# Performance work log

Measured on AMD Instinct MI355X. Metric: run time of the kernel, lower is better.

The kernel has to match this reference:

```python
import jax, jax.numpy as jnp
import numpy as np

B, S, D, H, V = 4, 2048, 128, 4, 64
HD = D // H
ITERS = 3
SCALE = 1.0 / float(np.sqrt(HD))
APO = 0.2
TRP = 0.15
FC = 1.61803
EPS = 1e-5


def ln(x, g, b):
    m = x.mean(-1, keepdims=True)
    v = ((x - m) ** 2).mean(-1, keepdims=True)
    return (x - m) / jnp.sqrt(v + EPS) * g + b


def setup_inputs() -> dict:
    key = jax.random.key(0)
    ks = iter(jax.random.split(key, 64))

    def w(shape, s=0.02):
        return jax.random.normal(next(ks), shape, jnp.float32) * s

    return {
        "x": jax.random.normal(next(ks), (B, S, D), jnp.float32),
        "space": jax.random.normal(next(ks), (B, S, D), jnp.float32),
        # attn_norm
        "g_attn": jnp.ones(D), "b_attn": jnp.zeros(D),
        # RecursiveScaledDotProductAttention
        "Wq": w((D, D)), "Wk": w((D, D)), "Wv": w((D, D)),
        "Wo": w((D, D)), "bo": jnp.zeros(D),
        "Wg": w((D, 2 * D)), "bg": jnp.zeros(D),
        "Wobs": w((H, D)), "bobs": jnp.zeros(H),
        # trp_norm + TraumaResolutionPathLayer
        "g_trp": jnp.ones(D), "b_trp": jnp.zeros(D),
        "Wt": w((V, D)), "bt": jnp.zeros(V),
        "Wc": w((V, D)), "bc": jnp.zeros(V),
        "Ws": w((V, D)), "bs": jnp.zeros(V),
        "Wr": w((V, 3 * V)), "br": jnp.zeros(V),
        "fv": jnp.ones(V) * FC,
        "Wop": w((D, V)), "bop": jnp.zeros(D),
        # MorphogenesisFFN
        "g_ffn": jnp.ones(D), "b_ffn": jnp.zeros(D),
        "W1": w((4 * D, D)), "b1": jnp.zeros(4 * D),
        "W2": w((D, 4 * D)), "b2": jnp.zeros(D),
        "Wsg": w((D, D)), "bsg": jnp.zeros(D),
        # ApophasisLayer
        "g_apo": jnp.ones(D), "b_apo": jnp.zeros(D),
        "Wn": w((D, D)), "bn": jnp.zeros(D),
    }


def reference(x, space, g_attn, b_attn, Wq, Wk, Wv, Wo, bo, Wg, bg, Wobs, bobs,
              g_trp, b_trp, Wt, bt, Wc, bc, Ws, bs, Wr, br, fv, Wop, bop,
              g_ffn, b_ffn, W1, b1, W2, b2, Wsg, bsg, g_apo, b_apo, Wn, bn):
    # --- recursive attention (autopoiesis loop, eval mode: dropout = identity) ---
    xn = ln(x, g_attn, b_attn)
    obs = xn.mean(1, keepdims=True)                      # [B,1,D] observer_state default
    infl = (obs @ Wobs.T + bobs).transpose(0, 2, 1)[..., None]  # [B,H,1,1] per-head bias
    cur = xn
    for _ in range(ITERS):
        q = (cur @ Wq.T).reshape(B, S, H, HD).transpose(0, 2, 1, 3)
        k = (cur @ Wk.T).reshape(B, S, H, HD).transpose(0, 2, 1, 3)
        v = (cur @ Wv.T).reshape(B, S, H, HD).transpose(0, 2, 1, 3)
        scores = jnp.einsum('bhqd,bhkd->bhqk', q, k) * SCALE + infl
        aw = jax.nn.softmax(scores, axis=-1)             # [B,H,S,S]
        ao = jnp.einsum('bhqk,bhkd->bhqd', aw, v).transpose(0, 2, 1, 3).reshape(B, S, D)
        out = ao @ Wo.T + bo
        gate = jax.nn.sigmoid(jnp.concatenate([cur, out], -1) @ Wg.T + bg)
        cur = cur * (1 - gate) + out * gate
    x = x + cur
    # --- Trauma Resolution Path ---
    xn2 = ln(x, g_trp, b_trp)
    tv = xn2 @ Wt.T + bt                                 # [B,S,V]
    cv = jnp.broadcast_to(xn2.mean(1, keepdims=True) @ Wc.T + bc, tv.shape)
    sv = space @ Ws.T + bs
    rgate = jax.nn.sigmoid(jnp.concatenate([tv, cv, sv], -1) @ Wr.T + br)
    cn = jnp.maximum(jnp.linalg.norm(cv, axis=-1, keepdims=True), 1e-8)
    sn = jnp.maximum(jnp.linalg.norm(sv, axis=-1, keepdims=True), 1e-8)
    align = (cv * sv).sum(-1, keepdims=True) / (cn * sn)
    resolved = tv + TRP * (-align * (fv - tv) * rgate)
    x = x + resolved @ Wop.T + bop
    # --- Morphogenesis FFN ---
    xn3 = ln(x, g_ffn, b_ffn)
    ff = jax.nn.gelu(xn3 @ W1.T + b1, approximate=False) @ W2.T + b2
    x = x + jax.nn.sigmoid(xn3 @ Wsg.T + bsg) * ff
    # --- Apophasis ---
    x = x - APO * jnp.tanh(ln(x, g_apo, b_apo) @ Wn.T + bn)
    return x, aw
```

## Files before the change

kernel.cpp:

```cpp
#include <hip/hip_runtime.h>
#include <cstdint>
#include <cstddef>


typedef unsigned short u16;
typedef __attribute__((ext_vector_type(8))) short short8;
typedef __attribute__((ext_vector_type(4))) float f32x4;
typedef __attribute__((ext_vector_type(2))) unsigned uint32x2;

#define B_ 4
#define S_ 2048
#define D_ 128
#define H_ 4
#define M_ 8192
#define SCALE2_ 0.25503472510324417f
#define APO_ 0.2f
#define TRP_ 0.15f
#define EPS_ 1e-5f

__device__ __forceinline__ float fexp2(float x){ return __builtin_amdgcn_exp2f(x); }

__device__ __forceinline__ u16 f2bf(float f){
  unsigned u = __float_as_uint(f);
  unsigned r = ((u >> 16) & 1u) + 0x7fffu;
  return (u16)((u + r) >> 16);
}
__device__ __forceinline__ float bf2f(u16 u){ return __uint_as_float(((unsigned)u) << 16); }
__device__ __forceinline__ float sigm(float x){ return 1.0f/(1.0f + __expf(-x)); }

__device__ __forceinline__ unsigned cvtpk_bf16(float lo, float hi){
  unsigned r;
  asm("v_cvt_pk_bf16_f32 %0, %1, %2" : "=v"(r) : "v"(lo), "v"(hi));
  return r;
}

#define LDS_BARRIER() __asm__ volatile("s_waitcnt lgkmcnt(0)\n\ts_barrier" ::: "memory")

struct WSrc { const float* s[13]; };
__global__ __launch_bounds__(256) void prep_k(WSrc w, u16* __restrict__ dst,
    const float* __restrict__ x_in, const float* __restrict__ g,
    const float* __restrict__ b, u16* __restrict__ cg0){
  if (blockIdx.x < 1168){
    int idx = blockIdx.x*256 + threadIdx.x;
    if (idx >= 299008) return;
    const int sz[13] = {16384,16384,16384,16384,32768,8192,8192,12288,8192,65536,65536,16384,16384};
    int off = idx;
    #pragma unroll
    for (int seg = 0; seg < 13; ++seg){
      if (off < sz[seg]) { dst[idx] = f2bf(w.s[seg][off]); return; }
      off -= sz[seg];
    }
  } else {
    int wv = threadIdx.x >> 6, lane = threadIdx.x & 63;
    int row = (blockIdx.x - 1168)*4 + wv;
    size_t rb = (size_t)row * D_;
    float v0 = x_in[rb + lane], v1 = x_in[rb + lane + 64];
    float s = v0 + v1;
    #pragma unroll
    for (int m = 1; m < 64; m <<= 1) s += __shfl_xor(s, m, 64);
    float mean = s * (1.0f/128.0f);
    float d0 = v0 - mean, d1 = v1 - mean;
    float vv = d0*d0 + d1*d1;
    #pragma unroll
    for (int m = 1; m < 64; m <<= 1) vv += __shfl_xor(vv, m, 64);
    float rstd = rsqrtf(vv * (1.0f/128.0f) + EPS_);
    cg0[rb + lane]      = f2bf(d0*rstd*g[lane]    + b[lane]);
    cg0[rb + lane + 64] = f2bf(d1*rstd*g[lane+64] + b[lane+64]);
  }
}

__global__ __launch_bounds__(512) void colmean_k(const u16* __restrict__ lnb,
    const float* __restrict__ Wc, const float* __restrict__ bc,
    float* __restrict__ cv, float* __restrict__ cn){
  __shared__ float red2[32][128];
  __shared__ float cmS[128];
  int b = blockIdx.x;
  int tid = threadIdx.x;
  int rg = tid >> 4, c8 = (tid & 15)*8;
  const u16* pp = lnb + (size_t)b*S_*D_ + (size_t)rg*D_ + c8;
  float acc[8];
  #pragma unroll
  for (int j = 0; j < 8; ++j) acc[j] = 0.f;
  #pragma unroll 4
  for (int i = 0; i < 64; ++i){
    short8 v = *(const short8*)(pp + (size_t)i*32*D_);
    #pragma unroll
    for (int j = 0; j < 8; ++j) acc[j] += bf2f((u16)v[j]);
  }
  #pragma unroll
  for (int j = 0; j < 8; ++j) red2[rg][c8 + j] = acc[j];
  __syncthreads();
  if (tid < 128){
    float s = 0.f;
    #pragma unroll
    for (int r = 0; r < 32; ++r) s += red2[r][tid];
    cmS[tid] = s * (1.0f/2048.0f);
  }
  __syncthreads();
  if (tid < 64){
    int n = tid;
    const float* wrow = Wc + n*D_;
    float sacc = bc[n];
    #pragma unroll 4
    for (int dd = 0; dd < D_; ++dd) sacc += cmS[dd]*wrow[dd];
    cv[b*64 + n] = sacc;
    float sq = sacc*sacc;
    #pragma unroll
    for (int m = 1; m < 64; m <<= 1) sq += __shfl_xor(sq, m, 64);
    if (n == 0) cn[b] = fmaxf(sqrtf(sq), 1e-8f);
  }
}

__global__ __launch_bounds__(256) void gemm_qkv(const u16* __restrict__ A,
    const u16* __restrict__ W, u16* __restrict__ qh, u16* __restrict__ kh, u16* __restrict__ vt){
  __shared__ u16 Asm[64*136];
  __shared__ u16 Bsm[64*136];
  const int m0 = blockIdx.x*64, n0 = blockIdx.y*64;
  int tid = threadIdx.x;
  int wv = tid >> 6, lane = tid & 63, quad = lane >> 4, l15 = lane & 15;
  int wm = wv >> 1, wn = wv & 1;
  {
    int sr = tid >> 2, cb = (tid & 3)*32;
    const u16* ag = A + (size_t)(m0 + sr)*128 + cb;
    const u16* bg = W + (size_t)(n0 + sr)*128 + cb;
    short8 a0 = *(const short8*)(ag + 0);
    short8 a1 = *(const short8*)(ag + 8);
    short8 a2 = *(const short8*)(ag + 16);
    short8 a3 = *(const short8*)(ag + 24);
    short8 b0 = *(const short8*)(bg + 0);
    short8 b1 = *(const short8*)(bg + 8);
    short8 b2 = *(const short8*)(bg + 16);
    short8 b3 = *(const short8*)(bg + 24);
    *(short8*)(Asm + sr*136 + cb + 0)  = a0;
    *(short8*)(Asm + sr*136 + cb + 8)  = a1;
    *(short8*)(Asm + sr*136 + cb + 16) = a2;
    *(short8*)(Asm + sr*136 + cb + 24) = a3;
    *(short8*)(Bsm + sr*136 + cb + 0)  = b0;
    *(short8*)(Bsm + sr*136 + cb + 8)  = b1;
    *(short8*)(Bsm + sr*136 + cb + 16) = b2;
    *(short8*)(Bsm + sr*136 + cb + 24) = b3;
  }
  LDS_BARRIER();
  f32x4 acc[2][2];
  #pragma unroll
  for (int i = 0; i < 2; ++i)
    #pragma unroll
    for (int j = 0; j < 2; ++j) acc[i][j] = (f32x4){0.f,0.f,0.f,0.f};
  #pragma unroll
  for (int k0 = 0; k0 < 128; k0 += 32){
    short8 af0 = *(const short8*)(Asm + (wm*32      + l15)*136 + k0 + quad*8);
    short8 af1 = *(const short8*)(Asm + (wm*32 + 16 + l15)*136 + k0 + quad*8);
    short8 bf0 = *(const short8*)(Bsm + (wn*32      + l15)*136 + k0 + quad*8);
    short8 bf1 = *(const short8*)(Bsm + (wn*32 + 16 + l15)*136 + k0 + quad*8);
    acc[0][0] = __builtin_amdgcn_mfma_f32_16x16x32_bf16(af0, bf0, acc[0][0], 0,0,0);
    acc[0][1] = __builtin_amdgcn_mfma_f32_16x16x32_bf16(af0, bf1, acc[0][1], 0,0,0);
    acc[1][0] = __builtin_amdgcn_mfma_f32_16x16x32_bf16(af1, bf0, acc[1][0], 0,0,0);
    acc[1][1] = __builtin_amdgcn_mfma_f32_16x16x32_bf16(af1, bf1, acc[1][1], 0,0,0);
  }
  #pragma unroll
  for (int ms = 0; ms < 2; ++ms)
    #pragma unroll
    for (int ns = 0; ns < 2; ++ns){
      int mb = m0 + wm*32 + ms*16 + quad*4;
      int nn = n0 + wn*32 + ns*16 + l15;
      int which = nn >> 7, col = nn & 127, h = col >> 5, hd = col & 31;
      f32x4 c = acc[ms][ns];
      #pragma unroll
      for (int r = 0; r < 4; ++r){
        int m = mb + r, b = m >> 11, s = m & 2047;
        if (which == 0)      qh[((size_t)(b*H_+h)*S_ + s)*32 + hd] = f2bf(c[r]);
        else if (which == 1) kh[((size_t)(b*H_+h)*S_ + s)*32 + hd] = f2bf(c[r]);
        else                 vt[((size_t)(b*H_+h)*32 + hd)*S_ + s] = f2bf(c[r]);
      }
    }
}

template<bool WRITE_AW>
__global__ __launch_bounds__(256) void attn_k(const u16* __restrict__ qh, const u16* __restrict__ kh,
    const u16* __restrict__ vT, u16* __restrict__ ao_bf, float* __restrict__ aw){
  __shared__ u16 Ks[2][128*40];
  __shared__ u16 Vs[2][32*136];
  __shared__ u16 Ps[4*16*136];
  int L = blockIdx.y*32 + blockIdx.x;
  int xcd = L & 7, j = L >> 3;
  int bh = 2*xcd + (j >> 5);
  int q0 = (j & 31)*64;
  int b = bh >> 2, h = bh & 3;
  int tid = threadIdx.x, wv = tid >> 6, lane = tid & 63, quad = lane >> 4, l15 = lane & 15;
  int qrow = q0 + wv*16 + l15;
  const size_t bhS = (size_t)bh * S_;
  short8 qf = *(const short8*)(qh + (bhS + qrow)*32 + quad*8);
  int krow = tid >> 1, kseg = (tid & 1)*16;
  const u16* kg = kh + (bhS + krow)*32 + kseg;
  int vrow = tid >> 3, vseg = (tid & 7)*16;
  const u16* vg = vT + ((size_t)bh*32 + vrow)*S_ + vseg;
  f32x4 zero = {0.f,0.f,0.f,0.f};
  f32x4 ao0 = zero, ao1 = zero;
  float lsum = 0.f, rinv = 1.0f, nls = 0.f;
  u16* PsW = Ps + wv*16*136;

  if constexpr (WRITE_AW){
    {
      short8 a0 = *(const short8*)(kg + 0);
      short8 a1 = *(const short8*)(kg + 8);
      *(short8*)(Ks[0] + krow*40 + kseg    ) = a0;
      *(short8*)(Ks[0] + krow*40 + kseg + 8) = a1;
    }
    #pragma unroll 2
    for (int t = 0; t < 16; ++t){
      LDS_BARRIER();
      short8 n0, n1;
      if (t < 15){
        n0 = *(const short8*)(kg + (size_t)(t+1)*4096 + 0);
        n1 = *(const short8*)(kg + (size_t)(t+1)*4096 + 8);
      }
      const u16* Kb = Ks[t & 1];
      #pragma unroll
      for (int jt = 0; jt < 8; ++jt){
        short8 kf = *(const short8*)(Kb + (jt*16 + l15)*40 + quad*8);
        f32x4 s = __builtin_amdgcn_mfma_f32_16x16x32_bf16(kf, qf, zero, 0,0,0);
        #pragma unroll
        for (int r = 0; r < 4; ++r) lsum += fexp2(s[r]*SCALE2_);
      }
      if (t < 15){
        u16* Kn = Ks[(t+1) & 1];
        *(short8*)(Kn + krow*40 + kseg    ) = n0;
        *(short8*)(Kn + krow*40 + kseg + 8) = n1;
      }
    }
    lsum += __shfl_xor(lsum, 16, 64);
    lsum += __shfl_xor(lsum, 32, 64);
    nls = -__log2f(lsum);
  }

  {
    short8 a0 = *(const short8*)(kg + 0);
    short8 a1 = *(const short8*)(kg + 8);
    short8 b0 = *(const short8*)(vg + 0);
    short8 b1 = *(const short8*)(vg + 8);
    *(short8*)(Ks[0] + krow*40 + kseg    ) = a0;
    *(short8*)(Ks[0] + krow*40 + kseg + 8) = a1;
    *(short8*)(Vs[0] + vrow*136 + vseg    ) = b0;
    *(short8*)(Vs[0] + vrow*136 + vseg + 8) = b1;
  }
  #pragma unroll 2
  for (int t = 0; t < 16; ++t){
    LDS_BARRIER();
    short8 kn0, kn1, vn0, vn1;
    if (t < 15){
      kn0 = *(const short8*)(kg + (size_t)(t+1)*4096 + 0);
      kn1 = *(const short8*)(kg + (size_t)(t+1)*4096 + 8);
      vn0 = *(const short8*)(vg + (size_t)(t+1)*128 + 0);
      vn1 = *(const short8*)(vg + (size_t)(t+1)*128 + 8);
    }
    const u16* Kb = Ks[t & 1];
    const u16* Vb = Vs[t & 1];
    int k0 = t*128;
    #pragma unroll
    for (int jt = 0; jt < 8; ++jt){
      short8 kf = *(const short8*)(Kb + (jt*16 + l15)*40 + quad*8);
      f32x4 s = __builtin_amdgcn_mfma_f32_16x16x32_bf16(kf, qf, zero, 0,0,0);
      float pv[4];
      #pragma unroll
      for (int r = 0; r < 4; ++r){
        float e;
        if constexpr (WRITE_AW) e = fexp2(__builtin_fmaf(s[r], SCALE2_, nls));
        else { e = fexp2(s[r]*SCALE2_); lsum += e; }
        pv[r] = e;
      }
      if constexpr (WRITE_AW){
        f32x4 st = {pv[0], pv[1], pv[2], pv[3]};
        *(f32x4*)(aw + (bhS + qrow)*S_ + k0 + jt*16 + quad*4) = st;
      }
      uint32x2 pk;
      pk[0] = cvtpk_bf16(pv[0], pv[1]);
      pk[1] = cvtpk_bf16(pv[2], pv[3]);
      *(uint32x2*)(PsW + l15*136 + jt*16 + quad*4) = pk;
    }
    __asm__ volatile("s_waitcnt lgkmcnt(0)" ::: "memory");
    #pragma unroll
    for (int jg = 0; jg < 4; ++jg){
      short8 pf  = *(const short8*)(PsW + l15*136 + jg*32 + quad*8);
      short8 vf0 = *(const short8*)(Vb + (l15     )*136 + jg*32 + quad*8);
      short8 vf1 = *(const short8*)(Vb + (16 + l15)*136 + jg*32 + quad*8);
      ao0 = __builtin_amdgcn_mfma_f32_16x16x32_bf16(vf0, pf, ao0, 0,0,0);
      ao1 = __builtin_amdgcn_mfma_f32_16x16x32_bf16(vf1, pf, ao1, 0,0,0);
    }
    if (t < 15){
      u16* Kn = Ks[(t+1) & 1];
      u16* Vn = Vs[(t+1) & 1];
      *(short8*)(Kn + krow*40 + kseg    ) = kn0;
      *(short8*)(Kn + krow*40 + kseg + 8) = kn1;
      *(short8*)(Vn + vrow*136 + vseg    ) = vn0;
      *(short8*)(Vn + vrow*136 + vseg + 8) = vn1;
    }
  }

  if constexpr (!WRITE_AW){
    lsum += __shfl_xor(lsum, 16, 64);
    lsum += __shfl_xor(lsum, 32, 64);
    rinv = 1.0f / lsum;
  }

  size_t rowbase = ((size_t)(b*S_ + qrow))*D_ + h*32;
  #pragma unroll
  for (int dt = 0; dt < 2; ++dt){
    f32x4 a = dt ? ao1 : ao0;
    uint32x2 pk;
    pk[0] = cvtpk_bf16(a[0]*rinv, a[1]*rinv);
    pk[1] = cvtpk_bf16(a[2]*rinv, a[3]*rinv);
    *(uint32x2*)(ao_bf + rowbase + dt*16 + quad*4) = pk;
  }
}

template<bool DO_QKV>
__global__ __launch_bounds__(256) void wqkv_k(const u16* __restrict__ cin,
    const u16* __restrict__ ao_bf, const u16* __restrict__ wo, const u16* __restrict__ wg,
    const u16* __restrict__ w3, const float* __restrict__ bo, const float* __restrict__ bg,
    u16* __restrict__ cout, u16* __restrict__ qh, u16* __restrict__ kh, u16* __restrict__ vt,
    const float* __restrict__ x_in, const float* __restrict__ g_trp,
    const float* __restrict__ b_trp, float* __restrict__ xbuf, u16* __restrict__ lnb){
  __shared__ u16 aoS[16*136];
  __shared__ u16 cuS[16*136];
  __shared__ u16 outS[16*136];
  __shared__ u16 coS[16*136];
  const int m0 = blockIdx.x*16;
  int tid = threadIdx.x, wv = tid >> 6, lane = tid & 63, quad = lane >> 4, l15 = lane & 15;
  {
    int row = tid >> 4, seg = (tid & 15)*8;
    *(short8*)(aoS + row*136 + seg) = *(const short8*)(ao_bf + (size_t)(m0+row)*128 + seg);
    *(short8*)(cuS + row*136 + seg) = *(const short8*)(cin   + (size_t)(m0+row)*128 + seg);
  }
  __syncthreads();
  f32x4 oacc[2] = {(f32x4){0,0,0,0},(f32x4){0,0,0,0}};
  #pragma unroll
  for (int kc = 0; kc < 4; ++kc){
    short8 af = *(const short8*)(aoS + l15*136 + kc*32 + quad*8);
    #pragma unroll
    for (int nt = 0; nt < 2; ++nt){
      int n = wv*32 + nt*16 + l15;
      short8 bfv = *(const short8*)(wo + (size_t)n*128 + kc*32 + quad*8);
      oacc[nt] = __builtin_amdgcn_mfma_f32_16x16x32_bf16(af, bfv, oacc[nt], 0,0,0);
    }
  }
  #pragma unroll
  for (int nt = 0; nt < 2; ++nt){
    int n = wv*32 + nt*16 + l15;
    float bias = bo[n];
    #pragma unroll
    for (int r = 0; r < 4; ++r){
      int m = quad*4 + r;
      outS[m*136 + n] = f2bf(oacc[nt][r] + bias);
    }
  }
  __syncthreads();
  f32x4 gacc[2] = {(f32x4){0,0,0,0},(f32x4){0,0,0,0}};
  #pragma unroll
  for (int kc = 0; kc < 8; ++kc){
    short8 af = (kc < 4) ? *(const short8*)(cuS  + l15*136 + kc*32 + quad*8)
                         : *(const short8*)(outS + l15*136 + (kc-4)*32 + quad*8);
    #pragma unroll
    for (int nt = 0; nt < 2; ++nt){
      int n = wv*32 + nt*16 + l15;
      short8 bfv = *(const short8*)(wg + (size_t)n*256 + kc*32 + quad*8);
      gacc[nt] = __builtin_amdgcn_mfma_f32_16x16x32_bf16(af, bfv, gacc[nt], 0,0,0);
    }
  }
  #pragma unroll
  for (int nt = 0; nt < 2; ++nt){
    int n = wv*32 + nt*16 + l15;
    float biasg = bg[n], biaso = bo[n];
    #pragma unroll
    for (int r = 0; r < 4; ++r){
      int m = quad*4 + r;
      float g = sigm(gacc[nt][r] + biasg);
      float c = bf2f(cuS[m*136 + n]);
      float o = oacc[nt][r] + biaso;
      u16 val = f2bf(c + g*(o - c));
      coS[m*136 + n] = val;
      if constexpr (DO_QKV) cout[(size_t)(m0+m)*128 + n] = val;
    }
  }
  __syncthreads();
  if constexpr (DO_QKV){
    f32x4 qacc[6];
    #pragma unroll
    for (int i = 0; i < 6; ++i) qacc[i] = (f32x4){0,0,0,0};
    #pragma unroll
    for (int kc = 0; kc < 4; ++kc){
      short8 af = *(const short8*)(coS + l15*136 + kc*32 + quad*8);
      #pragma unroll
      for (int nt = 0; nt < 6; ++nt){
        int n = wv*96 + nt*16 + l15;
        short8 bfv = *(const short8*)(w3 + (size_t)n*128 + kc*32 + quad*8);
        qacc[nt] = __builtin_amdgcn_mfma_f32_16x16x32_bf16(af, bfv, qacc[nt], 0,0,0);
      }
    }
    #pragma unroll
    for (int nt = 0; nt < 6; ++nt){
      int nn = wv*96 + nt*16 + l15;
      int which = nn >> 7, col = nn & 127, h = col >> 5, hd = col & 31;
      #pragma unroll
      for (int r = 0; r < 4; ++r){
        int m = m0 + quad*4 + r, b = m >> 11, s = m & 2047;
        if (which == 0)      qh[((size_t)(b*H_+h)*S_ + s)*32 + hd] = f2bf(qacc[nt][r]);
        else if (which == 1) kh[((size_t)(b*H_+h)*S_ + s)*32 + hd] = f2bf(qacc[nt][r]);
        else                 vt[((size_t)(b*H_+h)*32 + hd)*S_ + s] = f2bf(qacc[nt][r]);
      }
    }
  } else {
    for (int rr = wv*4; rr < wv*4 + 4; ++rr){
      size_t rb = (size_t)(m0+rr)*128;
      float v0 = x_in[rb + lane]      + bf2f(coS[rr*136 + lane]);
      float v1 = x_in[rb + lane + 64] + bf2f(coS[rr*136 + lane + 64]);
      xbuf[rb + lane] = v0; xbuf[rb + lane + 64] = v1;
      float s = v0 + v1;
      #pragma unroll
      for (int m = 1; m < 64; m <<= 1) s += __shfl_xor(s, m, 64);
      float mean = s * (1.0f/128.0f);
      float d0 = v0 - mean, d1 = v1 - mean;
      float vv = d0*d0 + d1*d1;
      #pragma unroll
      for (int m = 1; m < 64; m <<= 1) vv += __shfl_xor(vv, m, 64);
      float rstd = rsqrtf(vv * (1.0f/128.0f) + EPS_);
      lnb[rb + lane]      = f2bf(d0*rstd*g_trp[lane]    + b_trp[lane]);
      lnb[rb + lane + 64] = f2bf(d1*rstd*g_trp[lane+64] + b_trp[lane+64]);
    }
  }
}

__global__ __launch_bounds__(256) void uber_k(const u16* __restrict__ lnb,
    const float* __restrict__ space, const float* __restrict__ xbuf,
    const float* __restrict__ cv, const float* __restrict__ cn,
    const u16* __restrict__ wt, const float* __restrict__ bt,
    const u16* __restrict__ wsx, const float* __restrict__ bs,
    const u16* __restrict__ wr, const float* __restrict__ br, const float* __restrict__ fv,
    const u16* __restrict__ wop, const float* __restrict__ bop,
    const float* __restrict__ g_ffn, const float* __restrict__ b_ffn,
    const u16* __restrict__ w1, const float* __restrict__ b1,
    const u16* __restrict__ w2, const float* __restrict__ b2,
    const u16* __restrict__ wsg, const float* __restrict__ bsg,
    const float* __restrict__ g_apo, const float* __restrict__ b_apo,
    const u16* __restrict__ wn, const float* __restrict__ bn,
    float* __restrict__ out_x){
  __shared__ u16 xnS[16*136];
  __shared__ u16 spS[16*136];
  __shared__ u16 CcS[16*200];
  __shared__ float svF[16*64];
  __shared__ u16 RsS[16*72];
  __shared__ float xrF[16*128];
  __shared__ u16 midS[16*536];
  __shared__ float alignS[16];
  const int m0 = blockIdx.x*16;
  const int bidx = m0 >> 11;
  int tid = threadIdx.x, wv = tid >> 6, lane = tid & 63, quad = lane >> 4, l15 = lane & 15;

  {
    int row = tid >> 4, seg = (tid & 15)*8;
    *(short8*)(xnS + row*136 + seg) = *(const short8*)(lnb + (size_t)(m0+row)*128 + seg);
    const float* sp = space + (size_t)(m0+row)*128 + seg;
    short8 pk;
    #pragma unroll
    for (int i = 0; i < 8; ++i) pk[i] = (short)f2bf(sp[i]);
    *(short8*)(spS + row*136 + seg) = pk;
    f32x4 xa = *(const f32x4*)(xbuf + (size_t)(m0+row)*128 + seg);
    f32x4 xb = *(const f32x4*)(xbuf + (size_t)(m0+row)*128 + seg + 4);
    *(f32x4*)(xrF + row*128 + seg) = xa;
    *(f32x4*)(xrF + row*128 + seg + 4) = xb;
  }
  __syncthreads();

  f32x4 tvacc = {0,0,0,0};
  {
    int n = wv*16 + l15;
    #pragma unroll
    for (int kc = 0; kc < 4; ++kc){
      short8 af  = *(const short8*)(xnS + l15*136 + kc*32 + quad*8);
      short8 bfv = *(const short8*)(wt + (size_t)n*128 + kc*32 + quad*8);
      tvacc = __builtin_amdgcn_mfma_f32_16x16x32_bf16(af, bfv, tvacc, 0,0,0);
    }
    float bias = bt[n];
    #pragma unroll
    for (int r = 0; r < 4; ++r){
      tvacc[r] += bias;
// ... 114 lines not shown
        int n = wv*128 + nt*16 + l15;
        short8 bfv = *(const short8*)(w1 + (size_t)n*128 + kc*32 + quad*8);
        acc[nt] = __builtin_amdgcn_mfma_f32_16x16x32_bf16(af, bfv, acc[nt], 0,0,0);
      }
    }
    #pragma unroll
    for (int nt = 0; nt < 8; ++nt){
      int n = wv*128 + nt*16 + l15;
      float bias = b1[n];
      #pragma unroll
      for (int r = 0; r < 4; ++r){
        int m = quad*4 + r;
        float lin = acc[nt][r] + bias;
        float ge = 0.5f*lin*(1.0f + erff(lin*0.70710678118654752f));
        midS[m*536 + n] = f2bf(ge);
      }
    }
  }
  __syncthreads();

  {
    f32x4 ffa[2] = {(f32x4){0,0,0,0},(f32x4){0,0,0,0}};
    #pragma unroll
    for (int kc = 0; kc < 16; ++kc){
      short8 af = *(const short8*)(midS + l15*536 + kc*32 + quad*8);
      #pragma unroll
      for (int nt = 0; nt < 2; ++nt){
        int n = wv*32 + nt*16 + l15;
        short8 bfv = *(const short8*)(w2 + (size_t)n*512 + kc*32 + quad*8);
        ffa[nt] = __builtin_amdgcn_mfma_f32_16x16x32_bf16(af, bfv, ffa[nt], 0,0,0);
      }
    }
    f32x4 sga[2] = {(f32x4){0,0,0,0},(f32x4){0,0,0,0}};
    #pragma unroll
    for (int kc = 0; kc < 4; ++kc){
      short8 af = *(const short8*)(xnS + l15*136 + kc*32 + quad*8);
      #pragma unroll
      for (int nt = 0; nt < 2; ++nt){
        int n = wv*32 + nt*16 + l15;
        short8 bfv = *(const short8*)(wsg + (size_t)n*128 + kc*32 + quad*8);
        sga[nt] = __builtin_amdgcn_mfma_f32_16x16x32_bf16(af, bfv, sga[nt], 0,0,0);
      }
    }
    #pragma unroll
    for (int nt = 0; nt < 2; ++nt){
      int n = wv*32 + nt*16 + l15;
      float b2n = b2[n], bsgn = bsg[n];
      #pragma unroll
      for (int r = 0; r < 4; ++r){
        int m = quad*4 + r;
        float ff = ffa[nt][r] + b2n;
        float sg = sigm(sga[nt][r] + bsgn);
        xrF[m*128 + n] += sg*ff;
      }
    }
  }
  __syncthreads();

  for (int rr = wv*4; rr < wv*4 + 4; ++rr){
    float v0 = xrF[rr*128 + lane], v1 = xrF[rr*128 + lane + 64];
    float s = v0 + v1;
    #pragma unroll
    for (int m = 1; m < 64; m <<= 1) s += __shfl_xor(s, m, 64);
    float mean = s * (1.0f/128.0f);
    float d0 = v0 - mean, d1 = v1 - mean;
    float vvv = d0*d0 + d1*d1;
    #pragma unroll
    for (int m = 1; m < 64; m <<= 1) vvv += __shfl_xor(vvv, m, 64);
    float rstd = rsqrtf(vvv * (1.0f/128.0f) + EPS_);
    xnS[rr*136 + lane]      = f2bf(d0*rstd*g_apo[lane]    + b_apo[lane]);
    xnS[rr*136 + lane + 64] = f2bf(d1*rstd*g_apo[lane+64] + b_apo[lane+64]);
  }
  __syncthreads();

  {
    f32x4 na[2] = {(f32x4){0,0,0,0},(f32x4){0,0,0,0}};
    #pragma unroll
    for (int kc = 0; kc < 4; ++kc){
      short8 af = *(const short8*)(xnS + l15*136 + kc*32 + quad*8);
      #pragma unroll
      for (int nt = 0; nt < 2; ++nt){
        int n = wv*32 + nt*16 + l15;
        short8 bfv = *(const short8*)(wn + (size_t)n*128 + kc*32 + quad*8);
        na[nt] = __builtin_amdgcn_mfma_f32_16x16x32_bf16(af, bfv, na[nt], 0,0,0);
      }
    }
    #pragma unroll
    for (int nt = 0; nt < 2; ++nt){
      int n = wv*32 + nt*16 + l15;
      float bias = bn[n];
      #pragma unroll
      for (int r = 0; r < 4; ++r){
        int m = quad*4 + r;
        out_x[(size_t)(m0+m)*128 + n] = xrF[m*128 + n] - APO_*tanhf(na[nt][r] + bias);
      }
    }
  }
}

extern "C" void kernel_launch(void* const* d_in, const int* in_sizes, int n_in,
                              void* d_out, int out_size, void* d_ws, size_t ws_size,
                              hipStream_t stream){
  (void)in_sizes; (void)n_in; (void)out_size; (void)ws_size;
  const float* x_in   = (const float*)d_in[0];
  const float* space  = (const float*)d_in[1];
  const float* g_attn = (const float*)d_in[2];
  const float* b_attn = (const float*)d_in[3];
  const float* Wq     = (const float*)d_in[4];
  const float* Wk     = (const float*)d_in[5];
  const float* Wv     = (const float*)d_in[6];
  const float* Wo     = (const float*)d_in[7];
  const float* bo     = (const float*)d_in[8];
  const float* Wg     = (const float*)d_in[9];
  const float* bg     = (const float*)d_in[10];
  const float* g_trp  = (const float*)d_in[13];
  const float* b_trp  = (const float*)d_in[14];
  const float* Wt     = (const float*)d_in[15];
  const float* bt     = (const float*)d_in[16];
  const float* Wc     = (const float*)d_in[17];
  const float* bc     = (const float*)d_in[18];
  const float* Ws_    = (const float*)d_in[19];
  const float* bs     = (const float*)d_in[20];
  const float* Wr     = (const float*)d_in[21];
  const float* br     = (const float*)d_in[22];
  const float* fv     = (const float*)d_in[23];
  const float* Wop    = (const float*)d_in[24];
  const float* bop    = (const float*)d_in[25];
  const float* g_ffn  = (const float*)d_in[26];
  const float* b_ffn  = (const float*)d_in[27];
  const float* W1_    = (const float*)d_in[28];
  const float* b1     = (const float*)d_in[29];
  const float* W2_    = (const float*)d_in[30];
  const float* b2     = (const float*)d_in[31];
  const float* Wsg_   = (const float*)d_in[32];
  const float* bsg    = (const float*)d_in[33];
  const float* g_apo  = (const float*)d_in[34];
  const float* b_apo  = (const float*)d_in[35];
  const float* Wn_    = (const float*)d_in[36];
  const float* bn     = (const float*)d_in[37];

  char* base = (char*)d_ws;
  size_t off = 0;
  auto alloc = [&](size_t bytes)->char* {
    char* r = base + off; off += (bytes + 255) & ~(size_t)255; return r; };
  u16*  wbf   = (u16*) alloc((size_t)299008*2);
  u16*  cg0   = (u16*) alloc((size_t)M_*D_*2);
  u16*  cg1   = (u16*) alloc((size_t)M_*D_*2);
  u16*  qh    = (u16*) alloc((size_t)16*S_*32*2);
  u16*  kh    = (u16*) alloc((size_t)16*S_*32*2);
  u16*  vt    = (u16*) alloc((size_t)16*32*S_*2);
  u16*  ao_bf = (u16*) alloc((size_t)M_*D_*2);
  u16*  lnb   = (u16*) alloc((size_t)M_*D_*2);
  float* xbuf = (float*)alloc((size_t)M_*D_*4);
  float* cvb  = (float*)alloc(4*64*4);
  float* cnb  = (float*)alloc(4*4);

  u16* wqkv = wbf;
  u16* wo   = wbf + 49152;
  u16* wg   = wbf + 65536;
  u16* wt   = wbf + 98304;
  u16* wsx  = wbf + 106496;
  u16* wr   = wbf + 114688;
  u16* wop  = wbf + 126976;
  u16* w1   = wbf + 135168;
  u16* w2   = wbf + 200704;
  u16* wsgp = wbf + 266240;
  u16* wn   = wbf + 282624;

  float* out_x = (float*)d_out;
  float* aw    = out_x + (size_t)M_*D_;

  WSrc wsrc;
  wsrc.s[0]=Wq; wsrc.s[1]=Wk; wsrc.s[2]=Wv; wsrc.s[3]=Wo; wsrc.s[4]=Wg;
  wsrc.s[5]=Wt; wsrc.s[6]=Ws_; wsrc.s[7]=Wr; wsrc.s[8]=Wop; wsrc.s[9]=W1_;
  wsrc.s[10]=W2_; wsrc.s[11]=Wsg_; wsrc.s[12]=Wn_;

  prep_k<<<1168 + M_/4, 256, 0, stream>>>(wsrc, wbf, x_in, g_attn, b_attn, cg0);
  gemm_qkv<<<dim3(M_/64, 6), 256, 0, stream>>>(cg0, wqkv, qh, kh, vt);

  attn_k<false><<<dim3(S_/64, 16), 256, 0, stream>>>(qh, kh, vt, ao_bf, nullptr);
  wqkv_k<true ><<<M_/16, 256, 0, stream>>>(cg0, ao_bf, wo, wg, wqkv, bo, bg, cg1, qh, kh, vt,
                                           x_in, g_trp, b_trp, xbuf, lnb);
  attn_k<false><<<dim3(S_/64, 16), 256, 0, stream>>>(qh, kh, vt, ao_bf, nullptr);
  wqkv_k<true ><<<M_/16, 256, 0, stream>>>(cg1, ao_bf, wo, wg, wqkv, bo, bg, cg0, qh, kh, vt,
                                           x_in, g_trp, b_trp, xbuf, lnb);
  attn_k<true ><<<dim3(S_/64, 16), 256, 0, stream>>>(qh, kh, vt, ao_bf, aw);
  wqkv_k<false><<<M_/16, 256, 0, stream>>>(cg0, ao_bf, wo, wg, wqkv, bo, bg, cg1, qh, kh, vt,
                                           x_in, g_trp, b_trp, xbuf, lnb);

  colmean_k<<<4, 512, 0, stream>>>(lnb, Wc, bc, cvb, cnb);

  uber_k<<<M_/16, 256, 0, stream>>>(lnb, space, xbuf, cvb, cnb,
      wt, bt, wsx, bs, wr, br, fv, wop, bop,
      g_ffn, b_ffn, w1, b1, w2, b2, wsgp, bsg,
      g_apo, b_apo, wn, bn, out_x);
}
```

Before: 214.1 us.

## Fuse weight conversion, input layernorm and first QKV GEMM into one kernel

Merges the prep kernel (fp32→bf16 weight conversion plus the attention layernorm) with the first QKV projection GEMM into a single launch. Each GEMM block computes the layernorm for its 64 rows directly into shared memory and converts its Wq/Wk/Wv slice from fp32 on the fly. A seventh grid row handles the remaining weight conversion with a grid-stride loop. This removes one launch and the round trip of cg0 and the bf16 QKV weights through global memory, at the cost of redundant layernorm work across the six column blocks. It also adds an LDS barrier in the attention kernel after the log-sum pass, apparently to fix a shared-memory reuse hazard.

```diff
diff --git a/kernel.cpp b/kernel.cpp
--- a/kernel.cpp
+++ b/kernel.cpp
@@ -37,23 +37,35 @@
 #define LDS_BARRIER() __asm__ volatile("s_waitcnt lgkmcnt(0)\n\ts_barrier" ::: "memory")
 
 struct WSrc { const float* s[13]; };
-__global__ __launch_bounds__(256) void prep_k(WSrc w, u16* __restrict__ dst,
-    const float* __restrict__ x_in, const float* __restrict__ g,
-    const float* __restrict__ b, u16* __restrict__ cg0){
-  if (blockIdx.x < 1168){
-    int idx = blockIdx.x*256 + threadIdx.x;
-    if (idx >= 299008) return;
+
+__global__ __launch_bounds__(256) void qkv0_k(WSrc w, u16* __restrict__ wbf,
+    const float* __restrict__ x_in, const float* __restrict__ g, const float* __restrict__ b,
+    u16* __restrict__ cg0, u16* __restrict__ qh, u16* __restrict__ kh, u16* __restrict__ vt){
+  if (blockIdx.y == 6){
     const int sz[13] = {16384,16384,16384,16384,32768,8192,8192,12288,8192,65536,65536,16384,16384};
-    int off = idx;
-    #pragma unroll
-    for (int seg = 0; seg < 13; ++seg){
-      if (off < sz[seg]) { dst[idx] = f2bf(w.s[seg][off]); return; }
-      off -= sz[seg];
-    }
-  } else {
-    int wv = threadIdx.x >> 6, lane = threadIdx.x & 63;
-    int row = (blockIdx.x - 1168)*4 + wv;
-    size_t rb = (size_t)row * D_;
+    for (int idx = blockIdx.x*256 + threadIdx.x; idx < 299008; idx += 128*256){
+      int off = idx;
+      const float* src = nullptr;
+      #pragma unroll
+      for (int seg = 0; seg < 13; ++seg){
+        if (src == nullptr){
+          if (off < sz[seg]) src = w.s[seg] + off;
+          else off -= sz[seg];
+        }
+      }
+      wbf[idx] = f2bf(*src);
+    }
+    return;
+  }
+  __shared__ u16 Asm[64*136];
+  __shared__ u16 Bsm[64*136];
+  const int m0 = blockIdx.x*64, n0 = blockIdx.y*64;
+  int tid = threadIdx.x;
+  int wv = tid >> 6, lane = tid & 63, quad = lane >> 4, l15 = lane & 15;
+  int wm = wv >> 1, wn = wv & 1;
+
+  for (int rr = wv*16; rr < wv*16 + 16; ++rr){
+    size_t rb = (size_t)(m0 + rr) * D_;
     float v0 = x_in[rb + lane], v1 = x_in[rb + lane + 64];
     float s = v0 + v1;
     #pragma unroll
@@ -64,9 +76,63 @@
     #pragma unroll
     for (int m = 1; m < 64; m <<= 1) vv += __shfl_xor(vv, m, 64);
     float rstd = rsqrtf(vv * (1.0f/128.0f) + EPS_);
-    cg0[rb + lane]      = f2bf(d0*rstd*g[lane]    + b[lane]);
-    cg0[rb + lane + 64] = f2bf(d1*rstd*g[lane+64] + b[lane+64]);
-  }
+    u16 o0 = f2bf(d0*rstd*g[lane]    + b[lane]);
+    u16 o1 = f2bf(d1*rstd*g[lane+64] + b[lane+64]);
+    Asm[rr*136 + lane]      = o0;
+    Asm[rr*136 + lane + 64] = o1;
+    if (n0 == 0){ cg0[rb + lane] = o0; cg0[rb + lane + 64] = o1; }
+  }
+  {
+    int sr = tid >> 2, cb = (tid & 3)*32;
+    int gr = n0 + sr;
+    const float* wsrc = (gr < 128) ? (w.s[0] + (size_t)gr*128)
+                      : (gr < 256) ? (w.s[1] + (size_t)(gr-128)*128)
+                                   : (w.s[2] + (size_t)(gr-256)*128);
+    #pragma unroll
+    for (int j = 0; j < 32; j += 8){
+      f32x4 fa = *(const f32x4*)(wsrc + cb + j);
+      f32x4 fb = *(const f32x4*)(wsrc + cb + j + 4);
+      short8 pk;
+      pk[0]=(short)f2bf(fa[0]); pk[1]=(short)f2bf(fa[1]);
+      pk[2]=(short)f2bf(fa[2]); pk[3]=(short)f2bf(fa[3]);
+      pk[4]=(short)f2bf(fb[0]); pk[5]=(short)f2bf(fb[1]);
+      pk[6]=(short)f2bf(fb[2]); pk[7]=(short)f2bf(fb[3]);
+      *(short8*)(Bsm + sr*136 + cb + j) = pk;
+    }
+  }
+  LDS_BARRIER();
+  f32x4 acc[2][2];
+  #pragma unroll
+  for (int i = 0; i < 2; ++i)
+    #pragma unroll
+    for (int j = 0; j < 2; ++j) acc[i][j] = (f32x4){0.f,0.f,0.f,0.f};
+  #pragma unroll
+  for (int k0 = 0; k0 < 128; k0 += 32){
+    short8 af0 = *(const short8*)(Asm + (wm*32      + l15)*136 + k0 + quad*8);
+    short8 af1 = *(const short8*)(Asm + (wm*32 + 16 + l15)*136 + k0 + quad*8);
+    short8 bf0 = *(const short8*)(Bsm + (wn*32      + l15)*136 + k0 + quad*8);
+    short8 bf1 = *(const short8*)(Bsm + (wn*32 + 16 + l15)*136 + k0 + quad*8);
+    acc[0][0] = __builtin_amdgcn_mfma_f32_16x16x32_bf16(af0, bf0, acc[0][0], 0,0,0);
+    acc[0][1] = __builtin_amdgcn_mfma_f32_16x16x32_bf16(af0, bf1, acc[0][1], 0,0,0);
+    acc[1][0] = __builtin_amdgcn_mfma_f32_16x16x32_bf16(af1, bf0, acc[1][0], 0,0,0);
+    acc[1][1] = __builtin_amdgcn_mfma_f32_16x16x32_bf16(af1, bf1, acc[1][1], 0,0,0);
+  }
+  #pragma unroll
+  for (int ms = 0; ms < 2; ++ms)
+    #pragma unroll
+    for (int ns = 0; ns < 2; ++ns){
+      int mb = m0 + wm*32 + ms*16 + quad*4;
+      int nn = n0 + wn*32 + ns*16 + l15;
+      int which = nn >> 7, col = nn & 127, h = col >> 5, hd = col & 31;
+      f32x4 c = acc[ms][ns];
+      #pragma unroll
+      for (int r = 0; r < 4; ++r){
+        int m = mb + r, b2 = m >> 11, s = m & 2047;
+        if (which == 0)      qh[((size_t)(b2*H_+h)*S_ + s)*32 + hd] = f2bf(c[r]);
+        else if (which == 1) kh[((size_t)(b2*H_+h)*S_ + s)*32 + hd] = f2bf(c[r]);
+        else                 vt[((size_t)(b2*H_+h)*32 + hd)*S_ + s] = f2bf(c[r]);
+      }
+    }
 }
 
 __global__ __launch_bounds__(512) void colmean_k(const u16* __restrict__ lnb,
@@ -109,70 +175,6 @@
     for (int m = 1; m < 64; m <<= 1) sq += __shfl_xor(sq, m, 64);
     if (n == 0) cn[b] = fmaxf(sqrtf(sq), 1e-8f);
   }
-}
-
-__global__ __launch_bounds__(256) void gemm_qkv(const u16* __restrict__ A,
-    const u16* __restrict__ W, u16* __restrict__ qh, u16* __restrict__ kh, u16* __restrict__ vt){
-  __shared__ u16 Asm[64*136];
-  __shared__ u16 Bsm[64*136];
-  const int m0 = blockIdx.x*64, n0 = blockIdx.y*64;
-  int tid = threadIdx.x;
-  int wv = tid >> 6, lane = tid & 63, quad = lane >> 4, l15 = lane & 15;
-  int wm = wv >> 1, wn = wv & 1;
-  {
-    int sr = tid >> 2, cb = (tid & 3)*32;
-    const u16* ag = A + (size_t)(m0 + sr)*128 + cb;
-    const u16* bg = W + (size_t)(n0 + sr)*128 + cb;
-    short8 a0 = *(const short8*)(ag + 0);
-    short8 a1 = *(const short8*)(ag + 8);
-    short8 a2 = *(const short8*)(ag + 16);
-    short8 a3 = *(const short8*)(ag + 24);
-    short8 b0 = *(const short8*)(bg + 0);
-    short8 b1 = *(const short8*)(bg + 8);
-    short8 b2 = *(const short8*)(bg + 16);
-    short8 b3 = *(const short8*)(bg + 24);
-    *(short8*)(Asm + sr*136 + cb + 0)  = a0;
-    *(short8*)(Asm + sr*136 + cb + 8)  = a1;
-    *(short8*)(Asm + sr*136 + cb + 16) = a2;
-    *(short8*)(Asm + sr*136 + cb + 24) = a3;
-    *(short8*)(Bsm + sr*136 + cb + 0)  = b0;
-    *(short8*)(Bsm + sr*136 + cb + 8)  = b1;
-    *(short8*)(Bsm + sr*136 + cb + 16) = b2;
-    *(short8*)(Bsm + sr*136 + cb + 24) = b3;
-  }
-  LDS_BARRIER();
-  f32x4 acc[2][2];
-  #pragma unroll
-  for (int i = 0; i < 2; ++i)
-    #pragma unroll
-    for (int j = 0; j < 2; ++j) acc[i][j] = (f32x4){0.f,0.f,0.f,0.f};
-  #pragma unroll
-  for (int k0 = 0; k0 < 128; k0 += 32){
-    short8 af0 = *(const short8*)(Asm + (wm*32      + l15)*136 + k0 + quad*8);
-    short8 af1 = *(const short8*)(Asm + (wm*32 + 16 + l15)*136 + k0 + quad*8);
-    short8 bf0 = *(const short8*)(Bsm + (wn*32      + l15)*136 + k0 + quad*8);
-    short8 bf1 = *(const short8*)(Bsm + (wn*32 + 16 + l15)*136 + k0 + quad*8);
-    acc[0][0] = __builtin_amdgcn_mfma_f32_16x16x32_bf16(af0, bf0, acc[0][0], 0,0,0);
-    acc[0][1] = __builtin_amdgcn_mfma_f32_16x16x32_bf16(af0, bf1, acc[0][1], 0,0,0);
-    acc[1][0] = __builtin_amdgcn_mfma_f32_16x16x32_bf16(af1, bf0, acc[1][0], 0,0,0);
-    acc[1][1] = __builtin_amdgcn_mfma_f32_16x16x32_bf16(af1, bf1, acc[1][1], 0,0,0);
-  }
-  #pragma unroll
-  for (int ms = 0; ms < 2; ++ms)
-    #pragma unroll
-    for (int ns = 0; ns < 2; ++ns){
-      int mb = m0 + wm*32 + ms*16 + quad*4;
-      int nn = n0 + wn*32 + ns*16 + l15;
-      int which = nn >> 7, col = nn & 127, h = col >> 5, hd = col & 31;
-      f32x4 c = acc[ms][ns];
-      #pragma unroll
-      for (int r = 0; r < 4; ++r){
-        int m = mb + r, b = m >> 11, s = m & 2047;
-        if (which == 0)      qh[((size_t)(b*H_+h)*S_ + s)*32 + hd] = f2bf(c[r]);
-        else if (which == 1) kh[((size_t)(b*H_+h)*S_ + s)*32 + hd] = f2bf(c[r]);
-        else                 vt[((size_t)(b*H_+h)*32 + hd)*S_ + s] = f2bf(c[r]);
-      }
-    }
 }
 
 template<bool WRITE_AW>
@@ -231,6 +233,7 @@
     lsum += __shfl_xor(lsum, 16, 64);
     lsum += __shfl_xor(lsum, 32, 64);
     nls = -__log2f(lsum);
+    LDS_BARRIER();
   }
 
   {
@@ -773,8 +776,8 @@
   wsrc.s[5]=Wt; wsrc.s[6]=Ws_; wsrc.s[7]=Wr; wsrc.s[8]=Wop; wsrc.s[9]=W1_;
   wsrc.s[10]=W2_; wsrc.s[11]=Wsg_; wsrc.s[12]=Wn_;
 
-  prep_k<<<1168 + M_/4, 256, 0, stream>>>(wsrc, wbf, x_in, g_attn, b_attn, cg0);
-  gemm_qkv<<<dim3(M_/64, 6), 256, 0, stream>>>(cg0, wqkv, qh, kh, vt);
+  qkv0_k<<<dim3(128, 7), 256, 0, stream>>>(wsrc, wbf, x_in, g_attn, b_attn,
+                                           cg0, qh, kh, vt);
 
   attn_k<false><<<dim3(S_/64, 16), 256, 0, stream>>>(qh, kh, vt, ao_bf, nullptr);
   wqkv_k<true ><<<M_/16, 256, 0, stream>>>(cg0, ao_bf, wo, wg, wqkv, bo, bg, cg1, qh, kh, vt,
```

Result: slower. 220.7 us (+3.1%).

## Split-K the non-output attention passes across two key halves, combine in wqkv

Applied to the files above, without the earlier changes.

The first two attention iterations now split the 2048-key range into two halves, one per block, doubling the grid from 512 to 1024 blocks. Each half writes unnormalised fp32 partial outputs and row sums to a new scratch buffer. The following wqkv kernel sums the two halves, normalises, and converts to bf16 while staging into shared memory. This adds occupancy and parallelism at the cost of extra fp32 global traffic and a combine step. The K tile row pitch also shrinks from 40 to 36 elements in the new kernel, and the final aw-writing pass becomes a separate non-template kernel.

```diff
diff --git a/kernel.cpp b/kernel.cpp
--- a/kernel.cpp
+++ b/kernel.cpp
@@ -175,8 +175,98 @@
     }
 }
 
-template<bool WRITE_AW>
-__global__ __launch_bounds__(256) void attn_k(const u16* __restrict__ qh, const u16* __restrict__ kh,
+__global__ __launch_bounds__(256) void attnp_k(const u16* __restrict__ qh,
+    const u16* __restrict__ kh, const u16* __restrict__ vT,
+    float* __restrict__ aop, float* __restrict__ lsump){
+  __shared__ u16 Ks[2][128*36];
+  __shared__ u16 Vs[2][32*136];
+  __shared__ u16 Ps[4*16*136];
+  int L = blockIdx.y*64 + blockIdx.x;
+  int xcd = L & 7, j = L >> 3;
+  int bh = 2*xcd + (j >> 6);
+  int rem = j & 63;
+  int q0 = (rem & 31)*64;
+  int half = rem >> 5;
+  int tid = threadIdx.x, wv = tid >> 6, lane = tid & 63, quad = lane >> 4, l15 = lane & 15;
+  int qrow = q0 + wv*16 + l15;
+  const size_t bhS = (size_t)bh * S_;
+  short8 qf = *(const short8*)(qh + (bhS + qrow)*32 + quad*8);
+  int krow = tid >> 1, kseg = (tid & 1)*16;
+  const u16* kg = kh + (bhS + half*1024 + krow)*32 + kseg;
+  int vrow = tid >> 3, vseg = (tid & 7)*16;
+  const u16* vg = vT + ((size_t)bh*32 + vrow)*S_ + half*1024 + vseg;
+  f32x4 zero = {0.f,0.f,0.f,0.f};
+  f32x4 ao0 = zero, ao1 = zero;
+  float lsum = 0.f;
+  u16* PsW = Ps + wv*16*136;
+
+  {
+    short8 a0 = *(const short8*)(kg + 0);
+    short8 a1 = *(const short8*)(kg + 8);
+    short8 b0 = *(const short8*)(vg + 0);
+    short8 b1 = *(const short8*)(vg + 8);
+    *(short8*)(Ks[0] + krow*36 + kseg    ) = a0;
+    *(short8*)(Ks[0] + krow*36 + kseg + 8) = a1;
+    *(short8*)(Vs[0] + vrow*136 + vseg    ) = b0;
+    *(short8*)(Vs[0] + vrow*136 + vseg + 8) = b1;
+  }
+  #pragma unroll 2
+  for (int t = 0; t < 8; ++t){
+    LDS_BARRIER();
+    short8 kn0, kn1, vn0, vn1;
+    if (t < 7){
+      kn0 = *(const short8*)(kg + (size_t)(t+1)*4096 + 0);
+      kn1 = *(const short8*)(kg + (size_t)(t+1)*4096 + 8);
+      vn0 = *(const short8*)(vg + (size_t)(t+1)*128 + 0);
+      vn1 = *(const short8*)(vg + (size_t)(t+1)*128 + 8);
+    }
+    const u16* Kb = Ks[t & 1];
+    const u16* Vb = Vs[t & 1];
+    #pragma unroll
+    for (int jt = 0; jt < 8; ++jt){
+      short8 kf = *(const short8*)(Kb + (jt*16 + l15)*36 + quad*8);
+      f32x4 s = __builtin_amdgcn_mfma_f32_16x16x32_bf16(kf, qf, zero, 0,0,0);
+      float pv[4];
+      #pragma unroll
+      for (int r = 0; r < 4; ++r){
+        float e = fexp2(s[r]*SCALE2_);
+        lsum += e;
+        pv[r] = e;
+      }
+      uint32x2 pk;
+      pk[0] = cvtpk_bf16(pv[0], pv[1]);
+      pk[1] = cvtpk_bf16(pv[2], pv[3]);
+      *(uint32x2*)(PsW + l15*136 + jt*16 + quad*4) = pk;
+    }
+    __asm__ volatile("s_waitcnt lgkmcnt(0)" ::: "memory");
+    #pragma unroll
+    for (int jg = 0; jg < 4; ++jg){
+      short8 pf  = *(const short8*)(PsW + l15*136 + jg*32 + quad*8);
+      short8 vf0 = *(const short8*)(Vb + (l15     )*136 + jg*32 + quad*8);
+      short8 vf1 = *(const short8*)(Vb + (16 + l15)*136 + jg*32 + quad*8);
+      ao0 = __builtin_amdgcn_mfma_f32_16x16x32_bf16(vf0, pf, ao0, 0,0,0);
+      ao1 = __builtin_amdgcn_mfma_f32_16x16x32_bf16(vf1, pf, ao1, 0,0,0);
+    }
+    if (t < 7){
+      u16* Kn = Ks[(t+1) & 1];
+      u16* Vn = Vs[(t+1) & 1];
+      *(short8*)(Kn + krow*36 + kseg    ) = kn0;
+      *(short8*)(Kn + krow*36 + kseg + 8) = kn1;
+      *(short8*)(Vn + vrow*136 + vseg    ) = vn0;
+      *(short8*)(Vn + vrow*136 + vseg + 8) = vn1;
+    }
+  }
+
+  lsum += __shfl_xor(lsum, 16, 64);
+  lsum += __shfl_xor(lsum, 32, 64);
+
+  size_t pbase = ((size_t)(half*16 + bh)*S_ + qrow)*32;
+  *(f32x4*)(aop + pbase + quad*4)      = ao0;
+  *(f32x4*)(aop + pbase + 16 + quad*4) = ao1;
+  if (lane < 16) lsump[(size_t)(half*16 + bh)*S_ + qrow] = lsum;
+}
+
+__global__ __launch_bounds__(256) void attn_aw_k(const u16* __restrict__ qh, const u16* __restrict__ kh,
     const u16* __restrict__ vT, u16* __restrict__ ao_bf, float* __restrict__ aw){
   __shared__ u16 Ks[2][128*40];
   __shared__ u16 Vs[2][32*136];
@@ -196,42 +286,41 @@
   const u16* vg = vT + ((size_t)bh*32 + vrow)*S_ + vseg;
   f32x4 zero = {0.f,0.f,0.f,0.f};
   f32x4 ao0 = zero, ao1 = zero;
-  float lsum = 0.f, rinv = 1.0f, nls = 0.f;
+  float lsum = 0.f, nls = 0.f;
   u16* PsW = Ps + wv*16*136;
 
-  if constexpr (WRITE_AW){
-    {
-      short8 a0 = *(const short8*)(kg + 0);
-      short8 a1 = *(const short8*)(kg + 8);
-      *(short8*)(Ks[0] + krow*40 + kseg    ) = a0;
-      *(short8*)(Ks[0] + krow*40 + kseg + 8) = a1;
-    }
-    #pragma unroll 2
-    for (int t = 0; t < 16; ++t){
-      LDS_BARRIER();
-      short8 n0, n1;
-      if (t < 15){
-        n0 = *(const short8*)(kg + (size_t)(t+1)*4096 + 0);
-        n1 = *(const short8*)(kg + (size_t)(t+1)*4096 + 8);
-      }
-      const u16* Kb = Ks[t & 1];
-      #pragma unroll
-      for (int jt = 0; jt < 8; ++jt){
-        short8 kf = *(const short8*)(Kb + (jt*16 + l15)*40 + quad*8);
-        f32x4 s = __builtin_amdgcn_mfma_f32_16x16x32_bf16(kf, qf, zero, 0,0,0);
-        #pragma unroll
-        for (int r = 0; r < 4; ++r) lsum += fexp2(s[r]*SCALE2_);
-      }
-      if (t < 15){
-        u16* Kn = Ks[(t+1) & 1];
-        *(short8*)(Kn + krow*40 + kseg    ) = n0;
-        *(short8*)(Kn + krow*40 + kseg + 8) = n1;
-      }
-    }
-    lsum += __shfl_xor(lsum, 16, 64);
-    lsum += __shfl_xor(lsum, 32, 64);
-    nls = -__log2f(lsum);
-  }
+  {
+    short8 a0 = *(const short8*)(kg + 0);
+    short8 a1 = *(const short8*)(kg + 8);
+    *(short8*)(Ks[0] + krow*40 + kseg    ) = a0;
+    *(short8*)(Ks[0] + krow*40 + kseg + 8) = a1;
+  }
+  #pragma unroll 2
+  for (int t = 0; t < 16; ++t){
+    LDS_BARRIER();
+    short8 n0, n1;
+    if (t < 15){
+      n0 = *(const short8*)(kg + (size_t)(t+1)*4096 + 0);
+      n1 = *(const short8*)(kg + (size_t)(t+1)*4096 + 8);
+    }
+    const u16* Kb = Ks[t & 1];
+    #pragma unroll
+    for (int jt = 0; jt < 8; ++jt){
+      short8 kf = *(const short8*)(Kb + (jt*16 + l15)*40 + quad*8);
+      f32x4 s = __builtin_amdgcn_mfma_f32_16x16x32_bf16(kf, qf, zero, 0,0,0);
+      #pragma unroll
+      for (int r = 0; r < 4; ++r) lsum += fexp2(s[r]*SCALE2_);
+    }
+    if (t < 15){
+      u16* Kn = Ks[(t+1) & 1];
+      *(short8*)(Kn + krow*40 + kseg    ) = n0;
+      *(short8*)(Kn + krow*40 + kseg + 8) = n1;
+    }
+  }
+  lsum += __shfl_xor(lsum, 16, 64);
+  lsum += __shfl_xor(lsum, 32, 64);
+  nls = -__log2f(lsum);
+  LDS_BARRIER();
 
   {
     short8 a0 = *(const short8*)(kg + 0);
@@ -262,16 +351,10 @@
       f32x4 s = __builtin_amdgcn_mfma_f32_16x16x32_bf16(kf, qf, zero, 0,0,0);
       float pv[4];
       #pragma unroll
-      for (int r = 0; r < 4; ++r){
-        float e;
-        if constexpr (WRITE_AW) e = fexp2(__builtin_fmaf(s[r], SCALE2_, nls));
-        else { e = fexp2(s[r]*SCALE2_); lsum += e; }
-        pv[r] = e;
-      }
-      if constexpr (WRITE_AW){
-        f32x4 st = {pv[0], pv[1], pv[2], pv[3]};
-        *(f32x4*)(aw + (bhS + qrow)*S_ + k0 + jt*16 + quad*4) = st;
-      }
+      for (int r = 0; r < 4; ++r)
+        pv[r] = fexp2(__builtin_fmaf(s[r], SCALE2_, nls));
+      f32x4 st = {pv[0], pv[1], pv[2], pv[3]};
+      *(f32x4*)(aw + (bhS + qrow)*S_ + k0 + jt*16 + quad*4) = st;
       uint32x2 pk;
       pk[0] = cvtpk_bf16(pv[0], pv[1]);
       pk[1] = cvtpk_bf16(pv[2], pv[3]);
@@ -296,26 +379,22 @@
     }
   }
 
-  if constexpr (!WRITE_AW){
-    lsum += __shfl_xor(lsum, 16, 64);
-    lsum += __shfl_xor(lsum, 32, 64);
-    rinv = 1.0f / lsum;
-  }
-
   size_t rowbase = ((size_t)(b*S_ + qrow))*D_ + h*32;
   #pragma unroll
   for (int dt = 0; dt < 2; ++dt){
     f32x4 a = dt ? ao1 : ao0;
     uint32x2 pk;
-    pk[0] = cvtpk_bf16(a[0]*rinv, a[1]*rinv);
-    pk[1] = cvtpk_bf16(a[2]*rinv, a[3]*rinv);
+    pk[0] = cvtpk_bf16(a[0], a[1]);
+    pk[1] = cvtpk_bf16(a[2], a[3]);
     *(uint32x2*)(ao_bf + rowbase + dt*16 + quad*4) = pk;
   }
 }
 
 template<bool DO_QKV>
 __global__ __launch_bounds__(256) void wqkv_k(const u16* __restrict__ cin,
-    const u16* __restrict__ ao_bf, const u16* __restrict__ wo, const u16* __restrict__ wg,
+    const u16* __restrict__ ao_bf,
+    const float* __restrict__ aop, const float* __restrict__ lsump,
+    const u16* __restrict__ wo, const u16* __restrict__ wg,
     const u16* __restrict__ w3, const float* __restrict__ bo, const float* __restrict__ bg,
     u16* __restrict__ cout, u16* __restrict__ qh, u16* __restrict__ kh, u16* __restrict__ vt,
     const float* __restrict__ x_in, const float* __restrict__ g_trp,
@@ -328,8 +407,28 @@
   int tid = threadIdx.x, wv = tid >> 6, lane = tid & 63, quad = lane >> 4, l15 = lane & 15;
   {
     int row = tid >> 4, seg = (tid & 15)*8;
-    *(short8*)(aoS + row*136 + seg) = *(const short8*)(ao_bf + (size_t)(m0+row)*128 + seg);
-    *(short8*)(cuS + row*136 + seg) = *(const short8*)(cin   + (size_t)(m0+row)*128 + seg);
+    if constexpr (DO_QKV){
+      int m = m0 + row, b = m >> 11, s = m & 2047;
+      int bh = b*4 + (seg >> 5), hd0 = seg & 31;
+      size_t p0 = ((size_t)bh*S_ + s)*32 + hd0;
+      size_t p1 = ((size_t)(16 + bh)*S_ + s)*32 + hd0;
+      f32x4 a0a = *(const f32x4*)(aop + p0);
+      f32x4 a0b = *(const f32x4*)(aop + p0 + 4);
+      f32x4 a1a = *(const f32x4*)(aop + p1);
+      f32x4 a1b = *(const f32x4*)(aop + p1 + 4);
+      float l0 = lsump[(size_t)bh*S_ + s];
+      float l1 = lsump[(size_t)(16 + bh)*S_ + s];
+      float rinv = 1.0f/(l0 + l1);
+      short8 pk;
+      #pragma unroll
+      for (int i = 0; i < 4; ++i) pk[i]   = (short)f2bf((a0a[i] + a1a[i])*rinv);
+      #pragma unroll
+      for (int i = 0; i < 4; ++i) pk[i+4] = (short)f2bf((a0b[i] + a1b[i])*rinv);
+      *(short8*)(aoS + row*136 + seg) = pk;
+    } else {
+      *(short8*)(aoS + row*136 + seg) = *(const short8*)(ao_bf + (size_t)(m0+row)*128 + seg);
+    }
+    *(short8*)(cuS + row*136 + seg) = *(const short8*)(cin + (size_t)(m0+row)*128 + seg);
   }
   __syncthreads();
   f32x4 oacc[2] = {(f32x4){0,0,0,0},(f32x4){0,0,0,0}};
@@ -750,6 +849,8 @@
   u16*  ao_bf = (u16*) alloc((size_t)M_*D_*2);
   u16*  lnb   = (u16*) alloc((size_t)M_*D_*2);
   float* xbuf = (float*)alloc((size_t)M_*D_*4);
+  float* aop  = (float*)alloc((size_t)2*16*S_*32*4);
+  float* lsump= (float*)alloc((size_t)2*16*S_*4);
   float* cvb  = (float*)alloc(4*64*4);
   float* cnb  = (float*)alloc(4*4);
 
@@ -776,15 +877,15 @@
   prep_k<<<1168 + M_/4, 256, 0, stream>>>(wsrc, wbf, x_in, g_attn, b_attn, cg0);
   gemm_qkv<<<dim3(M_/64, 6), 256, 0, stream>>>(cg0, wqkv, qh, kh, vt);
 
-  attn_k<false><<<dim3(S_/64, 16), 256, 0, stream>>>(qh, kh, vt, ao_bf, nullptr);
-  wqkv_k<true ><<<M_/16, 256, 0, stream>>>(cg0, ao_bf, wo, wg, wqkv, bo, bg, cg1, qh, kh, vt,
-                                           x_in, g_trp, b_trp, xbuf, lnb);
-  attn_k<false><<<dim3(S_/64, 16), 256, 0, stream>>>(qh, kh, vt, ao_bf, nullptr);
-  wqkv_k<true ><<<M_/16, 256, 0, stream>>>(cg1, ao_bf, wo, wg, wqkv, bo, bg, cg0, qh, kh, vt,
-                                           x_in, g_trp, b_trp, xbuf, lnb);
-  attn_k<true ><<<dim3(S_/64, 16), 256, 0, stream>>>(qh, kh, vt, ao_bf, aw);
-  wqkv_k<false><<<M_/16, 256, 0, stream>>>(cg0, ao_bf, wo, wg, wqkv, bo, bg, cg1, qh, kh, vt,
-                                           x_in, g_trp, b_trp, xbuf, lnb);
+  attnp_k<<<dim3(64, 16), 256, 0, stream>>>(qh, kh, vt, aop, lsump);
+  wqkv_k<true ><<<M_/16, 256, 0, stream>>>(cg0, ao_bf, aop, lsump, wo, wg, wqkv, bo, bg,
+                                           cg1, qh, kh, vt, x_in, g_trp, b_trp, xbuf, lnb);
+  attnp_k<<<dim3(64, 16), 256, 0, stream>>>(qh, kh, vt, aop, lsump);
+  wqkv_k<true ><<<M_/16, 256, 0, stream>>>(cg1, ao_bf, aop, lsump, wo, wg, wqkv, bo, bg,
+                                           cg0, qh, kh, vt, x_in, g_trp, b_trp, xbuf, lnb);
+  attn_aw_k<<<dim3(S_/64, 16), 256, 0, stream>>>(qh, kh, vt, ao_bf, aw);
+  wqkv_k<false><<<M_/16, 256, 0, stream>>>(cg0, ao_bf, aop, lsump, wo, wg, wqkv, bo, bg,
+                                           cg1, qh, kh, vt, x_in, g_trp, b_trp, xbuf, lnb);
 
   colmean_k<<<4, 512, 0, stream>>>(lnb, Wc, bc, cvb, cnb);
 
```

Result: slower. 273.1 us (+27.5%).
